# Performance work log

Hardware: AMD Instinct MI355X
Metric: run time of the kernel (lower is better)

## Reference

```python
import jax, jax.numpy as jnp
import numpy as np

N = 50000
E = 600000
D = 128
H = 8
DH = D // H
SCALE = float(np.sqrt(DH))


def setup_inputs() -> dict:
    key = jax.random.key(0)
    ks = jax.random.split(key, 12)
    s = 1.0 / np.sqrt(D)
    return {
        "x": jax.random.normal(ks[0], (N, D), jnp.float32),
        "edge_index": jax.random.randint(ks[1], (2, E), 0, N, jnp.int64),
        "edge_attr": jax.random.normal(ks[2], (E,), jnp.float32),
        "Wq": jax.random.uniform(ks[3], (D, D), jnp.float32, -s, s),
        "bq": jax.random.uniform(ks[4], (D,), jnp.float32, -s, s),
        "Wk": jax.random.uniform(ks[5], (D, D), jnp.float32, -s, s),
        "bk": jax.random.uniform(ks[6], (D,), jnp.float32, -s, s),
        "Wv": jax.random.uniform(ks[7], (D, D), jnp.float32, -s, s),
        "bv": jax.random.uniform(ks[8], (D,), jnp.float32, -s, s),
        "Wo": jax.random.uniform(ks[9], (D, D), jnp.float32, -s, s),
        "bo": jax.random.uniform(ks[10], (D,), jnp.float32, -s, s),
    }


def reference(x, edge_index, edge_attr, Wq, bq, Wk, bk, Wv, bv, Wo, bo):
    # Projections -> [N, H, DH]
    Q = (x @ Wq + bq).reshape(N, H, DH)
    K = (x @ Wk + bk).reshape(N, H, DH)
    V = (x @ Wv + bv).reshape(N, H, DH)
    row, col = edge_index[0], edge_index[1]
    q_i = Q[row]   # [E, H, DH] gather by destination (source of softmax segment)
    k_j = K[col]
    v_j = V[col]
    scores = jnp.sum(q_i * k_j, axis=-1) / SCALE  # [E, H]
    scores = scores + edge_attr[:, None]          # edge_attr broadcast over heads
    # Segment softmax per row-node; max is taken over heads then per node (as original)
    edge_max = scores.max(axis=1)                                  # [E]
    node_max = jax.ops.segment_max(edge_max, row, num_segments=N)  # [N]
    s_exp = jnp.exp(scores - node_max[row][:, None])               # [E, H]
    s_sum = jax.ops.segment_sum(s_exp, row, num_segments=N)        # [N, H]
    attn = s_exp / (s_sum[row] + 1e-8)                             # [E, H]
    # (dropout is identity in eval mode)
    out = jax.ops.segment_sum(attn[:, :, None] * v_j, row, num_segments=N)  # [N, H, DH]
    out = out.reshape(N, D)
    return out @ Wo + bo
```

## Files before the change

kernel.cpp:

```cpp
#include <hip/hip_runtime.h>
#include <math.h>

#define N_NODES 50000
#define N_EDGES 600000
#define DIM 128
#define HEADS 8
#define GBLK 1563
#define NB1 586
#define L1E 1024

typedef _Float16 v8h __attribute__((ext_vector_type(8)));
typedef _Float16 v2h __attribute__((ext_vector_type(2)));
typedef float v16f __attribute__((ext_vector_type(16)));
typedef float v2f __attribute__((ext_vector_type(2)));

union v8h_u {
    v8h v;
    v2h p[4];
    _Float16 e[8];
};

__device__ __forceinline__ float e4m3_to_f32_sw(unsigned int b) {
    unsigned int s = b >> 7, E = (b >> 3) & 0xF, m = b & 7;
    float v = (E == 0) ? (float)m * 0.001953125f
                       : ldexpf(1.0f + (float)m * 0.125f, (int)E - 7);
    return s ? -v : v;
}

template <bool HI>
__device__ __forceinline__ v2f cvt2_f8(unsigned int w) {
#if __has_builtin(__builtin_amdgcn_cvt_pk_f32_fp8)
    return __builtin_amdgcn_cvt_pk_f32_fp8((int)w, HI);
#else
    v2f r;
    r[0] = e4m3_to_f32_sw((w >> (HI ? 16 : 0)) & 0xff);
    r[1] = e4m3_to_f32_sw((w >> (HI ? 24 : 8)) & 0xff);
    return r;
#endif
}

__device__ __forceinline__ unsigned char f32_to_e4m3(float v) {
#if __has_builtin(__builtin_amdgcn_cvt_pk_fp8_f32)
    return (unsigned char)(__builtin_amdgcn_cvt_pk_fp8_f32(v, v, 0, false) & 0xff);
#else
    float a = fabsf(v);
    unsigned char sgn = (v < 0.f) ? 0x80 : 0;
    if (!(a >= 0.0078125f)) {
        int m = (int)(a * 512.0f + 0.5f);
        if (m > 7) return sgn | 8;
        return sgn | (unsigned char)m;
    }
    if (a >= 448.0f) return sgn | 0x7e;
    int e;
    float fr = frexpf(a, &e);
    int mant = (int)(fr * 16.0f + 0.5f);
    int E = e + 6;
    if (mant == 16) { mant = 8; E++; }
    if (E >= 16) return sgn | 0x7e;
    return sgn | (unsigned char)((E << 3) | (mant - 8));
#endif
}

__global__ __launch_bounds__(256) void prep_hist(const float* __restrict__ Wq,
                                                 const float* __restrict__ Wk,
                                                 const float* __restrict__ Wv,
                                                 const float* __restrict__ Wo,
                                                 _Float16* __restrict__ Wfrag,
                                                 const int* __restrict__ rowi,
                                                 int* __restrict__ bh) {
    __shared__ int lh[256];
    if (blockIdx.x >= 64) {
        int b = blockIdx.x - 64;
        int t = threadIdx.x;
        lh[t] = 0;
        __syncthreads();
        int e0 = b * L1E + t;
#pragma unroll
        for (int k = 0; k < 4; k++) {
            int e = e0 + k * 256;
            if (e < N_EDGES) atomicAdd(lh + (rowi[e] >> 8), 1);
        }
        __syncthreads();
        bh[t * NB1 + b] = lh[t];
        return;
    }
    int i = blockIdx.x * 256 + threadIdx.x;
    int base = i * 4;
    int mat = i >> 12;
    int rem = i & 4095;
    int wave = rem >> 10;
    int kt = (rem >> 7) & 7;
    int lane = (rem >> 1) & 63;
    int jh = (rem & 1) * 4;
    const float* src = (mat == 0) ? Wq : (mat == 1) ? Wk : (mat == 2) ? Wv : Wo;
    int n = wave * 32 + (lane & 31);
    int kbase = kt * 16 + (lane >> 5) * 8 + jh;
    _Float16 o[4];
#pragma unroll
    for (int j = 0; j < 4; j++) o[j] = (_Float16)src[(kbase + j) * 128 + n];
    *(short4*)(Wfrag + base) = *(short4*)o;
}

#define LDSTRIDE 132
__global__ __launch_bounds__(256) void qkv_scan(const float* __restrict__ x,
                                                const _Float16* __restrict__ Wfrag,
                                                const float* __restrict__ bq,
                                                const float* __restrict__ bk,
                                                const float* __restrict__ bv,
                                                _Float16* __restrict__ Qh,
                                                unsigned char* __restrict__ K8,
                                                _Float16* __restrict__ Vh,
                                                const int* __restrict__ bh,
                                                int* __restrict__ within,
                                                int* __restrict__ dt) {
    __shared__ _Float16 As[32 * LDSTRIDE];
    __shared__ int sh[256];
    if (blockIdx.x >= GBLK) {
        int d = blockIdx.x - GBLK;
        int t = threadIdx.x;
        int carry = 0;
        for (int c = 0; c < 3; c++) {
            int j = c * 256 + t;
            int v = (j < NB1) ? bh[d * NB1 + j] : 0;
            __syncthreads();
            sh[t] = v;
            __syncthreads();
            for (int off = 1; off < 256; off <<= 1) {
                int a = sh[t];
                int b2 = (t >= off) ? sh[t - off] : 0;
                __syncthreads();
                sh[t] = a + b2;
                __syncthreads();
            }
            if (j < NB1) within[d * NB1 + j] = carry + sh[t] - v;
            carry += sh[255];
        }
        if (t == 0) dt[d] = carry;
        return;
    }
    int tid = threadIdx.x;
    int wave = tid >> 6, lane = tid & 63;
    int m32 = lane & 31, quad = lane >> 5;
    int row0 = blockIdx.x * 32;

    {
        int r = tid >> 3;
        int c0 = (tid & 7) * 16;
        int gr = row0 + r;
        bool valid = gr < N_NODES;
        const float4* src = (const float4*)(x + (size_t)gr * 128 + c0);
        _Float16* dst = As + r * LDSTRIDE + c0;
#pragma unroll
        for (int q = 0; q < 4; q++) {
            float4 v = valid ? src[q] : make_float4(0.f, 0.f, 0.f, 0.f);
            _Float16 o[4] = {(_Float16)v.x, (_Float16)v.y, (_Float16)v.z, (_Float16)v.w};
            *(short4*)(dst + q * 4) = *(short4*)o;
        }
    }
    __syncthreads();

    v8h af[8];
#pragma unroll
    for (int kt = 0; kt < 8; kt++)
        af[kt] = *(const v8h*)(As + m32 * LDSTRIDE + kt * 16 + quad * 8);

    int col = wave * 32 + m32;
#pragma unroll
    for (int mat = 0; mat < 3; mat++) {
        const _Float16* wf = Wfrag + mat * 16384 + wave * 4096 + lane * 8;
        v16f acc;
#pragma unroll
        for (int r = 0; r < 16; r++) acc[r] = 0.0f;
#pragma unroll
        for (int kt = 0; kt < 8; kt++) {
            v8h bf = *(const v8h*)(wf + kt * 512);
            acc = __builtin_amdgcn_mfma_f32_32x32x16_f16(af[kt], bf, acc, 0, 0, 0);
        }
        const float* bias = (mat == 0) ? bq : (mat == 1) ? bk : bv;
        float bias_v = bias[col];
        if (mat == 1) {
#pragma unroll
            for (int r = 0; r < 16; r++) {
                int row = (r & 3) + 8 * (r >> 2) + 4 * quad;
                int gr = row0 + row;
                if (gr < N_NODES) K8[(size_t)gr * 128 + col] = f32_to_e4m3(acc[r] + bias_v);
            }
        } else {
            _Float16* C = (mat == 0) ? Qh : Vh;
#pragma unroll
            for (int r = 0; r < 16; r++) {
                int row = (r & 3) + 8 * (r >> 2) + 4 * quad;
                int gr = row0 + row;
                if (gr < N_NODES) C[(size_t)gr * 128 + col] = (_Float16)(acc[r] + bias_v);
            }
        }
    }
}

__global__ __launch_bounds__(256) void l1scat(const int* __restrict__ rowi,
                                              const int* __restrict__ coli,
                                              const float* __restrict__ eattr,
                                              const int* __restrict__ within,
                                              const int* __restrict__ dt,
                                              unsigned long long* __restrict__ rec1) {
    __shared__ int lh[256], base[256], sh[256];
    int b = blockIdx.x, t = threadIdx.x;
    int v = dt[t];
    sh[t] = v;
    __syncthreads();
    for (int off = 1; off < 256; off <<= 1) {
        int a = sh[t];
        int b2 = (t >= off) ? sh[t - off] : 0;
        __syncthreads();
        sh[t] = a + b2;
        __syncthreads();
    }
    int dto = sh[t] - v;
    lh[t] = 0;
    base[t] = dto + within[t * NB1 + b];
    __syncthreads();
    int e0 = b * L1E + t;
#pragma unroll
    for (int k = 0; k < 4; k++) {
        int e = e0 + k * 256;
        if (e < N_EDGES) {
            int row = rowi[e];
            int d = row >> 8;
            int r = atomicAdd(lh + d, 1);
            unsigned short eb = __builtin_bit_cast(unsigned short, (_Float16)eattr[e]);
            rec1[base[d] + r] = (unsigned long long)row |
                                ((unsigned long long)(unsigned int)coli[e] << 16) |
                                ((unsigned long long)eb << 32);
        }
    }
}

__global__ __launch_bounds__(256) void l2sort(const unsigned long long* __restrict__ rec1,
                                              const int* __restrict__ dt,
                                              int* __restrict__ counts,
                                              int* __restrict__ start,
                                              unsigned int* __restrict__ ep4) {
    __shared__ int h[256], hs[256], r2[256], sh[256];
    int d = blockIdx.x, t = threadIdx.x;
    int v0 = dt[t];
    sh[t] = v0;
    __syncthreads();
    for (int off = 1; off < 256; off <<= 1) {
        int a = sh[t];
        int b2 = (t >= off) ? sh[t - off] : 0;
        __syncthreads();
        sh[t] = a + b2;
        __syncthreads();
    }
    int cnt = dt[d];
    int s = sh[d] - cnt;
    int e = s + cnt;
    __syncthreads();
    h[t] = 0;
    r2[t] = 0;
    __syncthreads();
    for (int i = s + t; i < e; i += 256) atomicAdd(h + (int)(rec1[i] & 255), 1);
    __syncthreads();
    int v = h[t];
    sh[t] = v;
    __syncthreads();
    for (int off = 1; off < 256; off <<= 1) {
        int a = sh[t];
        int b2 = (t >= off) ? sh[t - off] : 0;
        __syncthreads();
        sh[t] = a + b2;
        __syncthreads();
    }
    int ex = sh[t] - v;
    hs[t] = ex;
    int node = (d << 8) | t;
    if (node < N_NODES) {
        counts[node] = v;
        start[node] = s + ex;
    }
    __syncthreads();
    for (int i = s + t; i < e; i += 256) {
        unsigned long long w = rec1[i];
        int ld = (int)(w & 255);
        int r = atomicAdd(r2 + ld, 1);
        ep4[s + hs[ld] + r] = (unsigned int)(w >> 16);
    }
}

__global__ __launch_bounds__(256) void gemm_out(const _Float16* __restrict__ Ah,
                                                const _Float16* __restrict__ Wfrag,
                                                const float* __restrict__ bo,
                                                float* __restrict__ C) {
    __shared__ _Float16 As[32 * LDSTRIDE];
    int tid = threadIdx.x;
    int wave = tid >> 6, lane = tid & 63;
    int m32 = lane & 31, quad = lane >> 5;
    int row0 = blockIdx.x * 32;

    {
        int r = tid >> 3;
        int c0 = (tid & 7) * 16;
        int gr = row0 + r;
        bool valid = gr < N_NODES;
        const v8h* src = (const v8h*)(Ah + (size_t)gr * 128 + c0);
        _Float16* dst = As + r * LDSTRIDE + c0;
        v8h z = {};
        *(v8h*)(dst) = valid ? src[0] : z;
        *(v8h*)(dst + 8) = valid ? src[1] : z;
    }
    __syncthreads();

    v8h af[8];
#pragma unroll
    for (int kt = 0; kt < 8; kt++)
        af[kt] = *(const v8h*)(As + m32 * LDSTRIDE + kt * 16 + quad * 8);

    int col = wave * 32 + m32;
    const _Float16* wf = Wfrag + 3 * 16384 + wave * 4096 + lane * 8;
    v16f acc;
#pragma unroll
    for (int r = 0; r < 16; r++) acc[r] = 0.0f;
#pragma unroll
    for (int kt = 0; kt < 8; kt++) {
        v8h bf = *(const v8h*)(wf + kt * 512);
        acc = __builtin_amdgcn_mfma_f32_32x32x16_f16(af[kt], bf, acc, 0, 0, 0);
    }
    float bias_v = bo[col];
#pragma unroll
    for (int r = 0; r < 16; r++) {
        int row = (r & 3) + 8 * (r >> 2) + 4 * quad;
        int gr = row0 + row;
        if (gr < N_NODES) C[(size_t)gr * 128 + col] = acc[r] + bias_v;
    }
}

__global__ __launch_bounds__(256) void fused_attn(const _Float16* __restrict__ Q,
                                                  const unsigned char* __restrict__ K8,
                                                  const _Float16* __restrict__ V,
                                                  const int* __restrict__ start,
                                                  const int* __restrict__ counts,
                                                  const unsigned int* __restrict__ ep4,
                                                  _Float16* __restrict__ Aout) {
    int t = blockIdx.x * 256 + threadIdx.x;
    int n = t >> 4;
    int sub = t & 15;
    if (n >= N_NODES) return;

    int s0 = start[n];
    int cnt = counts[n];
    int e1 = s0 + cnt;

    v8h_u q;
    q.v = *(const v8h*)(Q + (size_t)n * 128 + sub * 8);
    float qf[8];
#pragma unroll
    for (int j = 0; j < 8; j++) qf[j] = (float)q.e[j];

    const unsigned char* Kb = K8 + sub * 8;
    const _Float16* Vb = V + sub * 8;

    float l = 0.0f;
    float acc[8];
#pragma unroll
    for (int j = 0; j < 8; j++) acc[j] = 0.0f;

    int nb = (cnt + 15) >> 4;
    for (int b = 0; b < nb; b++) {
        int base = s0 + (b << 4);
        int li = base + sub;
        if (li >= e1) li = e1 - 1;
        unsigned int pv = ep4[li];

#pragma unroll
        for (int h = 0; h < 2; h++) {
            int hb = h << 3;
            if (base + hb < e1) {
                int cols[8];
                float eas[8];
#pragma unroll
                for (int u = 0; u < 8; u++) {
                    unsigned int w = (unsigned int)__shfl((int)pv, hb + u, 16);
                    cols[u] = (int)(w & 0xffffu);
                    eas[u] = (float)__builtin_bit_cast(_Float16, (unsigned short)(w >> 16));
                }
                uint2 kw[8];
                v8h_u vv[8];
#pragma unroll
                for (int u = 0; u < 8; u++) {
                    kw[u] = *(const uint2*)(Kb + ((size_t)cols[u] << 7));
                    vv[u].v = *(const v8h*)(Vb + ((size_t)cols[u] << 7));
                }
                __builtin_amdgcn_sched_barrier(0);
#pragma unroll
                for (int u = 0; u < 8; u++) {
                    v2f k01 = cvt2_f8<false>(kw[u].x);
                    v2f k23 = cvt2_f8<true>(kw[u].x);
                    v2f k45 = cvt2_f8<false>(kw[u].y);
                    v2f k67 = cvt2_f8<true>(kw[u].y);
                    float dot = 0.0f;
                    dot = fmaf(qf[0], k01[0], dot);
                    dot = fmaf(qf[1], k01[1], dot);
                    dot = fmaf(qf[2], k23[0], dot);
                    dot = fmaf(qf[3], k23[1], dot);
                    dot = fmaf(qf[4], k45[0], dot);
                    dot = fmaf(qf[5], k45[1], dot);
                    dot = fmaf(qf[6], k67[0], dot);
                    dot = fmaf(qf[7], k67[1], dot);
                    dot += __shfl_xor(dot, 1);
                    float s = dot * 0.25f + eas[u];
                    bool valid = (base + hb + u) < e1;
                    float ex = valid ? __expf(s) : 0.0f;
                    l += ex;
#pragma unroll
                    for (int j = 0; j < 8; j++) acc[j] = fmaf(ex, (float)vv[u].e[j], acc[j]);
                }
            }
        }
    }

    float inv = 1.0f / (l + 1e-8f);
    _Float16 tmp[8];
#pragma unroll
    for (int j = 0; j < 8; j++) tmp[j] = (_Float16)(acc[j] * inv);
    *(v8h*)(Aout + (size_t)n * 128 + sub * 8) = *(v8h*)tmp;
}

extern "C" void kernel_launch(void* const* d_in, const int* in_sizes, int n_in,
                              void* d_out, int out_size, void* d_ws, size_t ws_size,
                              hipStream_t stream) {
    const float* x = (const float*)d_in[0];
    const int* ei = (const int*)d_in[1];
    const float* eattr = (const float*)d_in[2];
    const float* Wq = (const float*)d_in[3];
    const float* bq = (const float*)d_in[4];
    const float* Wk = (const float*)d_in[5];
    const float* bk = (const float*)d_in[6];
    const float* Wv = (const float*)d_in[7];
    const float* bv = (const float*)d_in[8];
    const float* Wo = (const float*)d_in[9];
    const float* bo = (const float*)d_in[10];
    float* out = (float*)d_out;

    const int* rowi = ei;
    const int* coli = ei + N_EDGES;

    _Float16* Qh = (_Float16*)d_ws;
    _Float16* Vh = Qh + (size_t)N_NODES * DIM;
    _Float16* Ah = Vh + (size_t)N_NODES * DIM;
    unsigned char* K8 = (unsigned char*)(Ah + (size_t)N_NODES * DIM);
    _Float16* Wfrag = (_Float16*)(K8 + (size_t)N_NODES * DIM);
    int* counts = (int*)(Wfrag + 4 * 16384);
    int* start = counts + N_NODES;
    int* bh = start + N_NODES;
    int* within = bh + 256 * NB1;
    int* dt = within + 256 * NB1;
    unsigned long long* rec1 = (unsigned long long*)(dt + 256);
    unsigned int* ep4 = (unsigned int*)(rec1 + N_EDGES);

    prep_hist<<<64 + NB1, 256, 0, stream>>>(Wq, Wk, Wv, Wo, Wfrag, rowi, bh);
    qkv_scan<<<GBLK + 256, 256, 0, stream>>>(x, Wfrag, bq, bk, bv, Qh, K8, Vh,
                                             bh, within, dt);
    l1scat<<<NB1, 256, 0, stream>>>(rowi, coli, eattr, within, dt, rec1);
    l2sort<<<196, 256, 0, stream>>>(rec1, dt, counts, start, ep4);
    int ablocks = (N_NODES * 16 + 255) / 256;
    fused_attn<<<ablocks, 256, 0, stream>>>(Qh, K8, Vh, start, counts, ep4, Ah);
    gemm_out<<<GBLK, 256, 0, stream>>>(Ah, Wfrag, bo, out);
}
```

Measured before the change: 177.7 us.

## Fuse output projection GEMM into attention kernel via LDS and 16x16 MFMA

Removes the separate gemm_out kernel and the fp16 intermediate attention buffer. Each attention block now processes 16 nodes, stages their normalized outputs in shared memory, and multiplies them by Wo using 16x16x32 MFMA. To match, the Wo fragment layout in prep is reordered. This saves one launch and an N×128 fp16 write and read round trip. In exchange it adds a block-wide barrier after the irregular per-node edge loops, so waves that finish early wait for the slowest node in their block.

```diff
diff --git a/kernel.cpp b/kernel.cpp
--- a/kernel.cpp
+++ b/kernel.cpp
@@ -12,6 +12,7 @@
 typedef _Float16 v8h __attribute__((ext_vector_type(8)));
 typedef _Float16 v2h __attribute__((ext_vector_type(2)));
 typedef float v16f __attribute__((ext_vector_type(16)));
+typedef float v4f __attribute__((ext_vector_type(4)));
 typedef float v2f __attribute__((ext_vector_type(2)));
 
 union v8h_u {
@@ -92,9 +93,17 @@
     int kt = (rem >> 7) & 7;
     int lane = (rem >> 1) & 63;
     int jh = (rem & 1) * 4;
-    const float* src = (mat == 0) ? Wq : (mat == 1) ? Wk : (mat == 2) ? Wv : Wo;
-    int n = wave * 32 + (lane & 31);
-    int kbase = kt * 16 + (lane >> 5) * 8 + jh;
+    int n, kbase;
+    const float* src;
+    if (mat == 3) {
+        src = Wo;
+        n = wave * 32 + ((kt >> 2) << 4) + (lane & 15);
+        kbase = (kt & 3) * 32 + ((lane >> 4) & 3) * 8 + jh;
+    } else {
+        src = (mat == 0) ? Wq : (mat == 1) ? Wk : Wv;
+        n = wave * 32 + (lane & 31);
+        kbase = kt * 16 + (lane >> 5) * 8 + jh;
+    }
     _Float16 o[4];
 #pragma unroll
     for (int j = 0; j < 4; j++) o[j] = (_Float16)src[(kbase + j) * 128 + n];
@@ -287,64 +296,21 @@
     }
 }
 
-__global__ __launch_bounds__(256) void gemm_out(const _Float16* __restrict__ Ah,
-                                                const _Float16* __restrict__ Wfrag,
-                                                const float* __restrict__ bo,
-                                                float* __restrict__ C) {
-    __shared__ _Float16 As[32 * LDSTRIDE];
-    int tid = threadIdx.x;
-    int wave = tid >> 6, lane = tid & 63;
-    int m32 = lane & 31, quad = lane >> 5;
-    int row0 = blockIdx.x * 32;
-
-    {
-        int r = tid >> 3;
-        int c0 = (tid & 7) * 16;
-        int gr = row0 + r;
-        bool valid = gr < N_NODES;
-        const v8h* src = (const v8h*)(Ah + (size_t)gr * 128 + c0);
-        _Float16* dst = As + r * LDSTRIDE + c0;
-        v8h z = {};
-        *(v8h*)(dst) = valid ? src[0] : z;
-        *(v8h*)(dst + 8) = valid ? src[1] : z;
-    }
-    __syncthreads();
-
-    v8h af[8];
-#pragma unroll
-    for (int kt = 0; kt < 8; kt++)
-        af[kt] = *(const v8h*)(As + m32 * LDSTRIDE + kt * 16 + quad * 8);
-
-    int col = wave * 32 + m32;
-    const _Float16* wf = Wfrag + 3 * 16384 + wave * 4096 + lane * 8;
-    v16f acc;
-#pragma unroll
-    for (int r = 0; r < 16; r++) acc[r] = 0.0f;
-#pragma unroll
-    for (int kt = 0; kt < 8; kt++) {
-        v8h bf = *(const v8h*)(wf + kt * 512);
-        acc = __builtin_amdgcn_mfma_f32_32x32x16_f16(af[kt], bf, acc, 0, 0, 0);
-    }
-    float bias_v = bo[col];
-#pragma unroll
-    for (int r = 0; r < 16; r++) {
-        int row = (r & 3) + 8 * (r >> 2) + 4 * quad;
-        int gr = row0 + row;
-        if (gr < N_NODES) C[(size_t)gr * 128 + col] = acc[r] + bias_v;
-    }
-}
-
 __global__ __launch_bounds__(256) void fused_attn(const _Float16* __restrict__ Q,
                                                   const unsigned char* __restrict__ K8,
                                                   const _Float16* __restrict__ V,
                                                   const int* __restrict__ start,
                                                   const int* __restrict__ counts,
                                                   const unsigned int* __restrict__ ep4,
-                                                  _Float16* __restrict__ Aout) {
-    int t = blockIdx.x * 256 + threadIdx.x;
-    int n = t >> 4;
-    int sub = t & 15;
-    if (n >= N_NODES) return;
+                                                  const _Float16* __restrict__ Wfrag,
+                                                  const float* __restrict__ bo,
+                                                  float* __restrict__ out) {
+    __shared__ _Float16 As16[16 * 132];
+    int tid = threadIdx.x;
+    int g = tid >> 4;
+    int sub = tid & 15;
+    int node_base = blockIdx.x * 16;
+    int n = node_base + g;
 
     int s0 = start[n];
     int cnt = counts[n];
@@ -422,7 +388,35 @@
     _Float16 tmp[8];
 #pragma unroll
     for (int j = 0; j < 8; j++) tmp[j] = (_Float16)(acc[j] * inv);
-    *(v8h*)(Aout + (size_t)n * 128 + sub * 8) = *(v8h*)tmp;
+
+    *(v8h*)(As16 + g * 132 + sub * 8) = *(v8h*)tmp;
+    __syncthreads();
+
+    {
+        int wave = tid >> 6, lane = tid & 63;
+        int lrow = lane & 15, lk = lane >> 4;
+        v8h af[4];
+#pragma unroll
+        for (int kk = 0; kk < 4; kk++)
+            af[kk] = *(const v8h*)(As16 + lrow * 132 + kk * 32 + lk * 8);
+        const _Float16* wofrag = Wfrag + 3 * 16384 + wave * 4096 + lane * 8;
+#pragma unroll
+        for (int c = 0; c < 2; c++) {
+            v4f acc2 = {0.f, 0.f, 0.f, 0.f};
+#pragma unroll
+            for (int kk = 0; kk < 4; kk++) {
+                v8h bf = *(const v8h*)(wofrag + (c * 4 + kk) * 512);
+                acc2 = __builtin_amdgcn_mfma_f32_16x16x32_f16(af[kk], bf, acc2, 0, 0, 0);
+            }
+            int col = wave * 32 + c * 16 + lrow;
+            float bias_v = bo[col];
+#pragma unroll
+            for (int r = 0; r < 4; r++) {
+                int node = node_base + lk * 4 + r;
+                out[(size_t)node * 128 + col] = acc2[r] + bias_v;
+            }
+        }
+    }
 }
 
 extern "C" void kernel_launch(void* const* d_in, const int* in_sizes, int n_in,
@@ -446,8 +440,7 @@
 
     _Float16* Qh = (_Float16*)d_ws;
     _Float16* Vh = Qh + (size_t)N_NODES * DIM;
-    _Float16* Ah = Vh + (size_t)N_NODES * DIM;
-    unsigned char* K8 = (unsigned char*)(Ah + (size_t)N_NODES * DIM);
+    unsigned char* K8 = (unsigned char*)(Vh + (size_t)N_NODES * DIM);
     _Float16* Wfrag = (_Float16*)(K8 + (size_t)N_NODES * DIM);
     int* counts = (int*)(Wfrag + 4 * 16384);
     int* start = counts + N_NODES;
@@ -462,7 +455,6 @@
                                              bh, within, dt);
     l1scat<<<NB1, 256, 0, stream>>>(rowi, coli, eattr, within, dt, rec1);
     l2sort<<<196, 256, 0, stream>>>(rec1, dt, counts, start, ep4);
-    int ablocks = (N_NODES * 16 + 255) / 256;
-    fused_attn<<<ablocks, 256, 0, stream>>>(Qh, K8, Vh, start, counts, ep4, Ah);
-    gemm_out<<<GBLK, 256, 0, stream>>>(Ah, Wfrag, bo, out);
-}
+    fused_attn<<<N_NODES / 16, 256, 0, stream>>>(Qh, K8, Vh, start, counts, ep4,
+                                                 Wfrag, bo, out);
+}
```

Measured after the change: 168.8 us. -5.0%, faster.
